# Kernel tuning notes

Hardware: AMD Instinct MI355X
Metric: run time of the kernel (lower is better)

Reference implementation:

```python
import jax, jax.numpy as jnp
import numpy as np

H = 256  # hidden_size


def _lstm_cell(x, h, c, Wih, Whh, b):
    # PyTorch gate order: input, forget, cell(g), output
    gates = x @ Wih.T + h @ Whh.T + b  # (B, 4H)
    i, f, g, o = jnp.split(gates, 4, axis=-1)
    c_new = jax.nn.sigmoid(f) * c + jax.nn.sigmoid(i) * jnp.tanh(g)
    h_new = jax.nn.sigmoid(o) * jnp.tanh(c_new)
    return h_new, c_new


def setup_inputs() -> dict:
    key = jax.random.key(0)
    ks = jax.random.split(key, 9)
    B, D_in, T, H4 = 64, 64, 1024, 4 * H
    s = 0.05  # keep gates out of saturation
    return {
        "x": jax.random.normal(ks[0], (B, D_in, T), jnp.float32),
        # layer 0: input size 64; layers 1-2: input size 2*H (bidirectional concat)
        "Wih0": jax.random.normal(ks[1], (2, H4, D_in), jnp.float32) * s,
        "Whh0": jax.random.normal(ks[2], (2, H4, H), jnp.float32) * s,
        "b0": jax.random.normal(ks[3], (2, H4), jnp.float32) * s,  # b_ih + b_hh fused
        "Wih12": jax.random.normal(ks[4], (2, 2, H4, 2 * H), jnp.float32) * s,
        "Whh12": jax.random.normal(ks[5], (2, 2, H4, H), jnp.float32) * s,
        "b12": jax.random.normal(ks[6], (2, 2, H4), jnp.float32) * s,
        # Conv1d(1, 81, (256,1)) == per-timestep linear over the hidden dim
        "conv_w": jax.random.normal(ks[7], (81, H), jnp.float32) * s,
        "conv_b": jax.random.normal(ks[8], (81,), jnp.float32) * s,
    }


def reference(x, Wih0, Whh0, b0, Wih12, Whh12, b12, conv_w, conv_b):
    B = x.shape[0]
    seq = jnp.transpose(x, (2, 0, 1))  # (T, B, D_in) like x.permute(2,0,1)
    h0 = jnp.zeros((6, B, H), x.dtype)  # num_layers * num_directions = 6
    c0 = jnp.zeros((6, B, H), x.dtype)

    def step(carry, x_t):
        h, c = carry
        hs, cs = [], []
        inp = x_t  # single timestep fed to the (bi)LSTM: both dirs see the same input
        for l in range(3):
            outs = []
            for d in range(2):
                idx = 2 * l + d
                if l == 0:
                    Wih, Whh, b = Wih0[d], Whh0[d], b0[d]
                else:
                    Wih, Whh, b = Wih12[l - 1, d], Whh12[l - 1, d], b12[l - 1, d]
                hn, cn = _lstm_cell(inp, h[idx], c[idx], Wih, Whh, b)
                outs.append(hn)
                hs.append(hn)
                cs.append(cn)
            inp = jnp.concatenate(outs, axis=-1)  # (B, 2H) into next layer
        new_h = jnp.stack(hs)
        new_c = jnp.stack(cs)
        # h.view(L, 2, B, H)[-1, -1]: last layer, backward direction
        return (new_h, new_c), hs[-1]

    _, ys = jax.lax.scan(step, (h0, c0), seq)  # ys: (T, B, H)

    # y.permute(1,2,0).unsqueeze(1) -> conv (256,1) kernel -> squeeze(2):
    # logits[b, o, t] = sum_h conv_w[o, h] * ys[t, b, h] + conv_b[o]
    logits = jnp.einsum('tbh,oh->bot', ys, conv_w) + conv_b[None, :, None]
    probs = jax.nn.softmax(logits, axis=1)
    return jnp.argmax(probs, axis=1)  # (B, T) int
```

## Files before the change

kernel.cpp:

```cpp
#include <hip/hip_runtime.h>


#define H_ 256
#define B_ 64
#define T_ 1024
#define NBLK 256
#define NTHR 1024
#define HBUF 98304
#define NTICK 1026

#define OFF_GEN  0
#define OFF_ROOT 64
#define OFF_CNT  128
#define OFF_H    4096
#define OFF_XT   1048576
#define OFF_YS   17825792

__device__ __forceinline__ float sigf(float x) {
  return 1.0f / (1.0f + __expf(-x));
}
__device__ __forceinline__ float tanhf_(float x) {
  float e = __expf(-2.0f * fabsf(x));
  float r = (1.0f - e) / (1.0f + e);
  return x >= 0.0f ? r : -r;
}

__device__ __forceinline__ void llc_ld1(const float4* p, float4& r) {
  asm volatile(
      "global_load_dwordx4 %0, %1, off sc0 sc1\n\t"
      "s_waitcnt vmcnt(0)"
      : "=v"(r)
      : "v"(p)
      : "memory");
}
__device__ __forceinline__ void llc_ld4(const float4* p, float4& r0, float4& r1,
                                        float4& r2, float4& r3) {
  asm volatile(
      "global_load_dwordx4 %0, %4, off sc0 sc1\n\t"
      "global_load_dwordx4 %1, %4, off offset:1024 sc0 sc1\n\t"
      "global_load_dwordx4 %2, %4, off offset:2048 sc0 sc1\n\t"
      "global_load_dwordx4 %3, %4, off offset:3072 sc0 sc1\n\t"
      "s_waitcnt vmcnt(0)"
      : "=&v"(r0), "=&v"(r1), "=&v"(r2), "=&v"(r3)
      : "v"(p)
      : "memory");
}
__device__ __forceinline__ void llc_ld8(const float4* p, const float4* q,
                                        float4& r0, float4& r1, float4& r2,
                                        float4& r3, float4& r4, float4& r5,
                                        float4& r6, float4& r7) {
  asm volatile(
      "global_load_dwordx4 %0, %8, off sc0 sc1\n\t"
      "global_load_dwordx4 %1, %8, off offset:1024 sc0 sc1\n\t"
      "global_load_dwordx4 %2, %8, off offset:2048 sc0 sc1\n\t"
      "global_load_dwordx4 %3, %8, off offset:3072 sc0 sc1\n\t"
      "global_load_dwordx4 %4, %9, off sc0 sc1\n\t"
      "global_load_dwordx4 %5, %9, off offset:1024 sc0 sc1\n\t"
      "global_load_dwordx4 %6, %9, off offset:2048 sc0 sc1\n\t"
      "global_load_dwordx4 %7, %9, off offset:3072 sc0 sc1\n\t"
      "s_waitcnt vmcnt(0)"
      : "=&v"(r0), "=&v"(r1), "=&v"(r2), "=&v"(r3), "=&v"(r4), "=&v"(r5),
        "=&v"(r6), "=&v"(r7)
      : "v"(p), "v"(q)
      : "memory");
}
__device__ __forceinline__ void llc_st_f2(float* p, float2 v) {
  asm volatile("global_store_dwordx2 %0, %1, off sc0 sc1" ::"v"(p), "v"(v)
               : "memory");
}

__global__ __launch_bounds__(64) void transpose_x(const float* __restrict__ x,
                                                  float* __restrict__ xT) {
  __shared__ float tile[64][65];
  const int k = blockIdx.y;
  const int t0 = blockIdx.x * 64;
  const int lane = threadIdx.x;
  for (int bi = 0; bi < 64; ++bi)
    tile[bi][lane] = x[bi * 65536 + k * 1024 + t0 + lane];
  __syncthreads();
  for (int ti = 0; ti < 64; ++ti)
    xT[(size_t)(t0 + ti) * 4096 + (k >> 2) * 256 + lane * 4 + (k & 3)] =
        tile[lane][ti];
}

__device__ __forceinline__ void body8(float* __restrict__ acc, const float4 av,
                                      const float* __restrict__ wl,
                                      const int k4) {
  const float* wp = wl + (size_t)k4 * 32;
#pragma unroll
  for (int a = 0; a < 8; ++a) {
    float4 wq = *(const float4*)(wp + a * 4);
    acc[a] += wq.x * av.x + wq.y * av.y + wq.z * av.z + wq.w * av.w;
  }
}

__device__ __forceinline__ void runLLC(float* __restrict__ acc,
                                       const float4* __restrict__ bufbase,
                                       const int bufk4, const int wk4,
                                       const int n,
                                       const float* __restrict__ wl,
                                       const int lane) {
  const float4* p = bufbase + (size_t)bufk4 * 64 + lane;
  int k = 0;
  for (; k + 8 <= n; k += 8) {
    float4 v0, v1, v2, v3, v4, v5, v6, v7;
    llc_ld8(p, p + 256, v0, v1, v2, v3, v4, v5, v6, v7);
    p += 512;
    body8(acc, v0, wl, wk4 + k + 0);
    body8(acc, v1, wl, wk4 + k + 1);
    body8(acc, v2, wl, wk4 + k + 2);
    body8(acc, v3, wl, wk4 + k + 3);
    body8(acc, v4, wl, wk4 + k + 4);
    body8(acc, v5, wl, wk4 + k + 5);
    body8(acc, v6, wl, wk4 + k + 6);
    body8(acc, v7, wl, wk4 + k + 7);
  }
  for (; k + 4 <= n; k += 4) {
    float4 v0, v1, v2, v3;
    llc_ld4(p, v0, v1, v2, v3);
    p += 256;
    body8(acc, v0, wl, wk4 + k + 0);
    body8(acc, v1, wl, wk4 + k + 1);
    body8(acc, v2, wl, wk4 + k + 2);
    body8(acc, v3, wl, wk4 + k + 3);
  }
  for (; k < n; ++k) {
    float4 v;
    llc_ld1(p, v);
    p += 64;
    body8(acc, v, wl, wk4 + k);
  }
}

__device__ __forceinline__ void runCached(float* __restrict__ acc,
                                          const float4* __restrict__ bufbase,
                                          const int bufk4, const int wk4,
                                          const int n,
                                          const float* __restrict__ wl,
                                          const int lane) {
  const float4* p = bufbase + (size_t)bufk4 * 64 + lane;
  int k = 0;
  for (; k + 4 <= n; k += 4) {
    float4 v0 = p[0], v1 = p[64], v2 = p[128], v3 = p[192];
    p += 256;
    body8(acc, v0, wl, wk4 + k + 0);
    body8(acc, v1, wl, wk4 + k + 1);
    body8(acc, v2, wl, wk4 + k + 2);
    body8(acc, v3, wl, wk4 + k + 3);
  }
  for (; k < n; ++k) {
    float4 v = *p;
    p += 64;
    body8(acc, v, wl, wk4 + k);
  }
}

__global__ __launch_bounds__(NTHR, 1) void lstm_persistent(
    const float* __restrict__ Wih0, const float* __restrict__ Whh0,
    const float* __restrict__ b0, const float* __restrict__ Wih12,
    const float* __restrict__ Whh12, const float* __restrict__ b12, char* wsb) {
  unsigned* gen = (unsigned*)(wsb + OFF_GEN);
  unsigned* root = (unsigned*)(wsb + OFF_ROOT);
  float* hb = (float*)(wsb + OFF_H);
  const float* xT = (const float*)(wsb + OFF_XT);
  float* ys = (float*)(wsb + OFF_YS);

  __shared__ float red[16][64][12];
  __shared__ float cst[3][2][64];
  __shared__ float wlds[14848];
  __shared__ float blds[3][8];

  const int bid = blockIdx.x;
  const int tid = threadIdx.x;
  const int lane = tid & 63;
  const int w = __builtin_amdgcn_readfirstlane(tid >> 6);
  const int d = bid >> 7;
  const int u0 = (bid & 127) * 2;

  if (tid < 384) ((float*)cst)[tid] = 0.f;

  auto stage = [&](const float* wA, int wAs, const float* wB, int wBs,
                   int K4s, int NA4s, float* dst) {
    const int nq = K4s * 8;
    for (int idx = tid; idx < nq; idx += NTHR) {
      const int a = idx / K4s;
      const int k4 = idx - a * K4s;
      const int row = (a & 3) * 256 + u0 + (a >> 2);
      const float* src = (k4 < NA4s) ? (wA + (size_t)row * wAs + k4 * 4)
                                     : (wB + (size_t)row * wBs + (k4 - NA4s) * 4);
      float4 q = *(const float4*)src;
      *(float4*)(dst + ((size_t)k4 * 8 + a) * 4) = q;
    }
  };
  stage(Wih0 + (size_t)d * 65536, 64, Whh0 + (size_t)d * 262144, 256, 80, 16,
        wlds);
  stage(Wih12 + (size_t)d * 524288, 512, Whh12 + (size_t)d * 262144, 256, 192,
        128, wlds + 2560);
  stage(Wih12 + (size_t)(2 + d) * 524288, 512,
        Whh12 + (size_t)(2 + d) * 262144, 256, 192, 128, wlds + 8704);
  if (tid < 24) {
    const int cell = tid >> 3, a = tid & 7;
    const float* bb = (cell == 0) ? (b0 + d * 1024)
                                  : ((cell == 1) ? (b12 + d * 1024)
                                                 : (b12 + (2 + d) * 1024));
    blds[cell][a] = bb[(a & 3) * 256 + u0 + (a >> 2)];
  }
  __syncthreads();

  unsigned* mycnt = (unsigned*)(wsb + OFF_CNT + (size_t)(bid & 7) * 64);

  for (unsigned tick = 0; tick < NTICK; ++tick) {
    const float* R = hb + ((tick + 1) & 1) * HBUF;
    float* W = hb + (tick & 1) * HBUF;
    const float4* Rf4 = (const float4*)R;

    const bool has0 = tick < 1024;
    const bool has1 = tick >= 1 && tick < 1025;
    const bool has2 = tick >= 2;

    float acc[8] = {0.f, 0.f, 0.f, 0.f, 0.f, 0.f, 0.f, 0.f};

    if (w < 4) {
      if (has0) {
        if (w == 0) {
          runCached(acc, (const float4*)xT + (size_t)tick * 1024, 0, 0, 16,
                    wlds, lane);
          runLLC(acc, Rf4 + (size_t)d * 4096, 0, 16, 4, wlds, lane);
        } else {
          const int lo = 20 * w;
          runLLC(acc, Rf4 + (size_t)d * 4096, lo - 16, lo, 20, wlds, lane);
        }
      }
    } else if (w < 10) {
      if (has1) {
        const int wi = w - 4, lo = 32 * wi;
        if (wi < 4)
          runLLC(acc, Rf4, lo, lo, 32, wlds + 2560, lane);
        else
          runLLC(acc, Rf4 + (size_t)(2 + d) * 4096, lo - 128, lo, 32,
                 wlds + 2560, lane);
      }
    } else {
      if (has2) {
        const int wi = w - 10, lo = 32 * wi;
        if (wi < 4)
          runLLC(acc, Rf4 + (size_t)2 * 4096, lo, lo, 32, wlds + 8704, lane);
        else
          runLLC(acc, Rf4 + (size_t)(4 + d) * 4096, lo - 128, lo, 32,
                 wlds + 8704, lane);
      }
    }

    *(float4*)&red[w][lane][0] = make_float4(acc[0], acc[1], acc[2], acc[3]);
    *(float4*)&red[w][lane][4] = make_float4(acc[4], acc[5], acc[6], acc[7]);
    __syncthreads();

    if (tid < 192) {
      const int cell = tid >> 6, b = tid & 63;
      const bool present = (cell == 0) ? has0 : ((cell == 1) ? has1 : has2);
      if (present) {
        const int w0 = (cell == 0) ? 0 : ((cell == 1) ? 4 : 10);
        const int nw = (cell == 0) ? 4 : 6;
        float g0 = blds[cell][0], g1 = blds[cell][1], g2 = blds[cell][2],
              g3 = blds[cell][3], g4 = blds[cell][4], g5 = blds[cell][5],
              g6 = blds[cell][6], g7 = blds[cell][7];
        for (int ww = w0; ww < w0 + nw; ++ww) {
          const float4* rp = (const float4*)&red[ww][b][0];
          float4 s0 = rp[0], s1 = rp[1];
          g0 += s0.x; g1 += s0.y; g2 += s0.z; g3 += s0.w;
          g4 += s1.x; g5 += s1.y; g6 += s1.z; g7 += s1.w;
        }
        const float iv0 = sigf(g0), fv0 = sigf(g1), gv0 = tanhf_(g2),
                    ov0 = sigf(g3);
        const float iv1 = sigf(g4), fv1 = sigf(g5), gv1 = tanhf_(g6),
                    ov1 = sigf(g7);
        float c0 = fv0 * cst[cell][0][b] + iv0 * gv0;
        float c1 = fv1 * cst[cell][1][b] + iv1 * gv1;
        cst[cell][0][b] = c0;
        cst[cell][1][b] = c1;
        const float h0 = ov0 * tanhf_(c0), h1 = ov1 * tanhf_(c1);
        const int cellidx = (cell == 0) ? d : ((cell == 1) ? (2 + d) : (4 + d));
        float* hp =
            W + (size_t)cellidx * 16384 + (u0 >> 2) * 256 + b * 4 + (u0 & 3);
        llc_st_f2(hp, make_float2(h0, h1));
        if (cell == 2 && d == 1) {
          *(float2*)(ys + (size_t)((int)tick - 2) * 16384 + b * 256 + u0) =
              make_float2(h0, h1);
        }
      }
    }
    asm volatile("s_waitcnt vmcnt(0)" ::: "memory");
    __syncthreads();

    if (tid == 0) {
      unsigned old = __hip_atomic_fetch_add(mycnt, 1u, __ATOMIC_RELAXED,
                                            __HIP_MEMORY_SCOPE_AGENT);
      if (old == (tick + 1) * (NBLK / 8) - 1) {
        unsigned r = __hip_atomic_fetch_add(root, 1u, __ATOMIC_RELAXED,
                                            __HIP_MEMORY_SCOPE_AGENT);
        if (r == (tick + 1) * 8 - 1) {
          __hip_atomic_store(gen, tick + 1, __ATOMIC_RELAXED,
                             __HIP_MEMORY_SCOPE_AGENT);
        }
      }
      while (__hip_atomic_load(gen, __ATOMIC_RELAXED, __HIP_MEMORY_SCOPE_AGENT) <
             tick + 1) {
        __builtin_amdgcn_s_sleep(2);
      }
    }
    __syncthreads();
  }
}

__global__ __launch_bounds__(256) void conv_argmax(const float* __restrict__ yst,
                                                   const float* __restrict__ cw,
                                                   const float* __restrict__ cb,
                                                   int* __restrict__ out) {
  const int t = blockIdx.x;
  const int tid = threadIdx.x, lane = tid & 63, w = tid >> 6;
  const float* yrow = yst + (size_t)t * (B_ * H_) + lane * H_;
  float best = -3.4e38f;
  int bi = 0;
  for (int og = 0; og < 3; ++og) {
    float acc[8];
    int ov[8];
#pragma unroll
    for (int m = 0; m < 8; ++m) {
      int o = w + 32 * og + 4 * m;
      ov[m] = (o < 81) ? o : 80;
      acc[m] = (o < 81) ? cb[o] : -3.4e38f;
    }
    for (int uu = 0; uu < H_; uu += 4) {
      float4 y4 = *(const float4*)(yrow + uu);
#pragma unroll
      for (int m = 0; m < 8; ++m) {
        const float* wr = cw + ov[m] * H_ + uu;
        acc[m] += wr[0] * y4.x + wr[1] * y4.y + wr[2] * y4.z + wr[3] * y4.w;
      }
    }
#pragma unroll
    for (int m = 0; m < 8; ++m) {
      int o = w + 32 * og + 4 * m;
      if (o < 81 && acc[m] > best) {
        best = acc[m];
        bi = o;
      }
    }
  }
  __shared__ float sv[4][64];
  __shared__ int si[4][64];
  sv[w][lane] = best;
  si[w][lane] = bi;
  __syncthreads();
  if (tid < 64) {
    float bv = sv[0][tid];
    int bo = si[0][tid];
#pragma unroll
    for (int ww = 1; ww < 4; ++ww) {
      float v = sv[ww][tid];
      int o = si[ww][tid];
      if (v > bv || (v == bv && o < bo)) {
        bv = v;
        bo = o;
      }
    }
    out[tid * T_ + t] = bo;
  }
}

extern "C" void kernel_launch(void* const* d_in, const int* in_sizes, int n_in,
                              void* d_out, int out_size, void* d_ws,
                              size_t ws_size, hipStream_t stream) {
  const float* x = (const float*)d_in[0];
  const float* Wih0 = (const float*)d_in[1];
  const float* Whh0 = (const float*)d_in[2];
  const float* b0 = (const float*)d_in[3];
  const float* Wih12 = (const float*)d_in[4];
  const float* Whh12 = (const float*)d_in[5];
  const float* b12 = (const float*)d_in[6];
  const float* cw = (const float*)d_in[7];
  const float* cb = (const float*)d_in[8];
  int* out = (int*)d_out;
  char* wsb = (char*)d_ws;

  hipMemsetAsync(wsb, 0, OFF_H + 786432, stream);
  transpose_x<<<dim3(16, 64, 1), dim3(64, 1, 1), 0, stream>>>(
      x, (float*)(wsb + OFF_XT));
  lstm_persistent<<<dim3(NBLK, 1, 1), dim3(NTHR, 1, 1), 0, stream>>>(
      Wih0, Whh0, b0, Wih12, Whh12, b12, wsb);
  conv_argmax<<<dim3(T_, 1, 1), dim3(256, 1, 1), 0, stream>>>(
      (const float*)(wsb + OFF_YS), cw, cb, out);
}
```

Measured before the change: 16.13 ms.

## Split LSTM persistent kernel into 512 blocks of one hidden unit each

Each persistent block now owns one hidden unit per direction instead of two. That doubles the grid to 512 blocks of 512 threads (8 waves) and halves per-block LDS weights, reduction buffers and cell state. Waves get longer K-ranges per cell, and the hierarchical barrier moves to 16 sub-counters. The intent is more blocks resident across CUs for parallelism and less per-block reduction work. The cost is that every block re-reads the full h vectors from LLC each tick, doubling global read traffic, and the grid barrier now has more participants.

Result: slower. 17.36 ms (+7.6%).

```diff
diff --git a/kernel.cpp b/kernel.cpp
--- a/kernel.cpp
+++ b/kernel.cpp
@@ -4,8 +4,8 @@
 #define H_ 256
 #define B_ 64
 #define T_ 1024
-#define NBLK 256
-#define NTHR 1024
+#define NBLK 512
+#define NTHR 512
 #define HBUF 98304
 #define NTICK 1026
 
@@ -64,8 +64,8 @@
       : "v"(p), "v"(q)
       : "memory");
 }
-__device__ __forceinline__ void llc_st_f2(float* p, float2 v) {
-  asm volatile("global_store_dwordx2 %0, %1, off sc0 sc1" ::"v"(p), "v"(v)
+__device__ __forceinline__ void llc_st1_nd(float* p, float v) {
+  asm volatile("global_store_dword %0, %1, off sc0 sc1" ::"v"(p), "v"(v)
                : "memory");
 }
 
@@ -83,12 +83,12 @@
         tile[lane][ti];
 }
 
-__device__ __forceinline__ void body8(float* __restrict__ acc, const float4 av,
+__device__ __forceinline__ void body4(float* __restrict__ acc, const float4 av,
                                       const float* __restrict__ wl,
                                       const int k4) {
-  const float* wp = wl + (size_t)k4 * 32;
-#pragma unroll
-  for (int a = 0; a < 8; ++a) {
+  const float* wp = wl + (size_t)k4 * 16;
+#pragma unroll
+  for (int a = 0; a < 4; ++a) {
     float4 wq = *(const float4*)(wp + a * 4);
     acc[a] += wq.x * av.x + wq.y * av.y + wq.z * av.z + wq.w * av.w;
   }
@@ -106,29 +106,29 @@
     float4 v0, v1, v2, v3, v4, v5, v6, v7;
     llc_ld8(p, p + 256, v0, v1, v2, v3, v4, v5, v6, v7);
     p += 512;
-    body8(acc, v0, wl, wk4 + k + 0);
-    body8(acc, v1, wl, wk4 + k + 1);
-    body8(acc, v2, wl, wk4 + k + 2);
-    body8(acc, v3, wl, wk4 + k + 3);
-    body8(acc, v4, wl, wk4 + k + 4);
-    body8(acc, v5, wl, wk4 + k + 5);
-    body8(acc, v6, wl, wk4 + k + 6);
-    body8(acc, v7, wl, wk4 + k + 7);
+    body4(acc, v0, wl, wk4 + k + 0);
+    body4(acc, v1, wl, wk4 + k + 1);
+    body4(acc, v2, wl, wk4 + k + 2);
+    body4(acc, v3, wl, wk4 + k + 3);
+    body4(acc, v4, wl, wk4 + k + 4);
+    body4(acc, v5, wl, wk4 + k + 5);
+    body4(acc, v6, wl, wk4 + k + 6);
+    body4(acc, v7, wl, wk4 + k + 7);
   }
   for (; k + 4 <= n; k += 4) {
     float4 v0, v1, v2, v3;
     llc_ld4(p, v0, v1, v2, v3);
     p += 256;
-    body8(acc, v0, wl, wk4 + k + 0);
-    body8(acc, v1, wl, wk4 + k + 1);
-    body8(acc, v2, wl, wk4 + k + 2);
-    body8(acc, v3, wl, wk4 + k + 3);
+    body4(acc, v0, wl, wk4 + k + 0);
+    body4(acc, v1, wl, wk4 + k + 1);
+    body4(acc, v2, wl, wk4 + k + 2);
+    body4(acc, v3, wl, wk4 + k + 3);
   }
   for (; k < n; ++k) {
     float4 v;
     llc_ld1(p, v);
     p += 64;
-    body8(acc, v, wl, wk4 + k);
+    body4(acc, v, wl, wk4 + k);
   }
 }
 
@@ -143,19 +143,19 @@
   for (; k + 4 <= n; k += 4) {
     float4 v0 = p[0], v1 = p[64], v2 = p[128], v3 = p[192];
     p += 256;
-    body8(acc, v0, wl, wk4 + k + 0);
-    body8(acc, v1, wl, wk4 + k + 1);
-    body8(acc, v2, wl, wk4 + k + 2);
-    body8(acc, v3, wl, wk4 + k + 3);
+    body4(acc, v0, wl, wk4 + k + 0);
+    body4(acc, v1, wl, wk4 + k + 1);
+    body4(acc, v2, wl, wk4 + k + 2);
+    body4(acc, v3, wl, wk4 + k + 3);
   }
   for (; k < n; ++k) {
     float4 v = *p;
     p += 64;
-    body8(acc, v, wl, wk4 + k);
-  }
-}
-
-__global__ __launch_bounds__(NTHR, 1) void lstm_persistent(
+    body4(acc, v, wl, wk4 + k);
+  }
+}
+
+__global__ __launch_bounds__(NTHR, 4) void lstm_persistent(
     const float* __restrict__ Wih0, const float* __restrict__ Whh0,
     const float* __restrict__ b0, const float* __restrict__ Wih12,
     const float* __restrict__ Whh12, const float* __restrict__ b12, char* wsb) {
@@ -165,49 +165,49 @@
   const float* xT = (const float*)(wsb + OFF_XT);
   float* ys = (float*)(wsb + OFF_YS);
 
-  __shared__ float red[16][64][12];
-  __shared__ float cst[3][2][64];
-  __shared__ float wlds[14848];
-  __shared__ float blds[3][8];
+  __shared__ float red[8][64][4];
+  __shared__ float cst[3][64];
+  __shared__ float wlds[7424];
+  __shared__ float blds[3][4];
 
   const int bid = blockIdx.x;
   const int tid = threadIdx.x;
   const int lane = tid & 63;
   const int w = __builtin_amdgcn_readfirstlane(tid >> 6);
-  const int d = bid >> 7;
-  const int u0 = (bid & 127) * 2;
-
-  if (tid < 384) ((float*)cst)[tid] = 0.f;
+  const int d = bid >> 8;
+  const int u = bid & 255;
+
+  if (tid < 192) ((float*)cst)[tid] = 0.f;
 
   auto stage = [&](const float* wA, int wAs, const float* wB, int wBs,
                    int K4s, int NA4s, float* dst) {
-    const int nq = K4s * 8;
+    const int nq = K4s * 4;
     for (int idx = tid; idx < nq; idx += NTHR) {
       const int a = idx / K4s;
       const int k4 = idx - a * K4s;
-      const int row = (a & 3) * 256 + u0 + (a >> 2);
+      const int row = a * 256 + u;
       const float* src = (k4 < NA4s) ? (wA + (size_t)row * wAs + k4 * 4)
                                      : (wB + (size_t)row * wBs + (k4 - NA4s) * 4);
       float4 q = *(const float4*)src;
-      *(float4*)(dst + ((size_t)k4 * 8 + a) * 4) = q;
+      *(float4*)(dst + ((size_t)k4 * 4 + a) * 4) = q;
     }
   };
   stage(Wih0 + (size_t)d * 65536, 64, Whh0 + (size_t)d * 262144, 256, 80, 16,
         wlds);
   stage(Wih12 + (size_t)d * 524288, 512, Whh12 + (size_t)d * 262144, 256, 192,
-        128, wlds + 2560);
+        128, wlds + 1280);
   stage(Wih12 + (size_t)(2 + d) * 524288, 512,
-        Whh12 + (size_t)(2 + d) * 262144, 256, 192, 128, wlds + 8704);
-  if (tid < 24) {
-    const int cell = tid >> 3, a = tid & 7;
+        Whh12 + (size_t)(2 + d) * 262144, 256, 192, 128, wlds + 4352);
+  if (tid < 12) {
+    const int cell = tid >> 2, a = tid & 3;
     const float* bb = (cell == 0) ? (b0 + d * 1024)
                                   : ((cell == 1) ? (b12 + d * 1024)
                                                  : (b12 + (2 + d) * 1024));
-    blds[cell][a] = bb[(a & 3) * 256 + u0 + (a >> 2)];
+    blds[cell][a] = bb[a * 256 + u];
   }
   __syncthreads();
 
-  unsigned* mycnt = (unsigned*)(wsb + OFF_CNT + (size_t)(bid & 7) * 64);
+  unsigned* mycnt = (unsigned*)(wsb + OFF_CNT + (size_t)(bid & 15) * 64);
 
   for (unsigned tick = 0; tick < NTICK; ++tick) {
     const float* R = hb + ((tick + 1) & 1) * HBUF;
@@ -218,74 +218,65 @@
     const bool has1 = tick >= 1 && tick < 1025;
     const bool has2 = tick >= 2;
 
-    float acc[8] = {0.f, 0.f, 0.f, 0.f, 0.f, 0.f, 0.f, 0.f};
-
-    if (w < 4) {
+    float acc[4] = {0.f, 0.f, 0.f, 0.f};
+
+    if (w < 2) {
       if (has0) {
         if (w == 0) {
           runCached(acc, (const float4*)xT + (size_t)tick * 1024, 0, 0, 16,
                     wlds, lane);
-          runLLC(acc, Rf4 + (size_t)d * 4096, 0, 16, 4, wlds, lane);
+          runLLC(acc, Rf4 + (size_t)d * 4096, 0, 16, 24, wlds, lane);
         } else {
-          const int lo = 20 * w;
-          runLLC(acc, Rf4 + (size_t)d * 4096, lo - 16, lo, 20, wlds, lane);
+          runLLC(acc, Rf4 + (size_t)d * 4096, 24, 40, 40, wlds, lane);
         }
       }
-    } else if (w < 10) {
+    } else if (w < 5) {
       if (has1) {
-        const int wi = w - 4, lo = 32 * wi;
-        if (wi < 4)
-          runLLC(acc, Rf4, lo, lo, 32, wlds + 2560, lane);
+        const int wi = w - 2;
+        if (wi < 2)
+          runLLC(acc, Rf4, wi * 64, wi * 64, 64, wlds + 1280, lane);
         else
-          runLLC(acc, Rf4 + (size_t)(2 + d) * 4096, lo - 128, lo, 32,
-                 wlds + 2560, lane);
+          runLLC(acc, Rf4 + (size_t)(2 + d) * 4096, 0, 128, 64, wlds + 1280,
+                 lane);
       }
     } else {
       if (has2) {
-        const int wi = w - 10, lo = 32 * wi;
-        if (wi < 4)
-          runLLC(acc, Rf4 + (size_t)2 * 4096, lo, lo, 32, wlds + 8704, lane);
+        const int wi = w - 5;
+        if (wi < 2)
+          runLLC(acc, Rf4 + (size_t)2 * 4096, wi * 64, wi * 64, 64,
+                 wlds + 4352, lane);
         else
-          runLLC(acc, Rf4 + (size_t)(4 + d) * 4096, lo - 128, lo, 32,
-                 wlds + 8704, lane);
+          runLLC(acc, Rf4 + (size_t)(4 + d) * 4096, 0, 128, 64, wlds + 4352,
+                 lane);
       }
     }
 
     *(float4*)&red[w][lane][0] = make_float4(acc[0], acc[1], acc[2], acc[3]);
-    *(float4*)&red[w][lane][4] = make_float4(acc[4], acc[5], acc[6], acc[7]);
     __syncthreads();
 
     if (tid < 192) {
       const int cell = tid >> 6, b = tid & 63;
       const bool present = (cell == 0) ? has0 : ((cell == 1) ? has1 : has2);
       if (present) {
-        const int w0 = (cell == 0) ? 0 : ((cell == 1) ? 4 : 10);
-        const int nw = (cell == 0) ? 4 : 6;
+        const int w0c = (cell == 0) ? 0 : ((cell == 1) ? 2 : 5);
+        const int nw = (cell == 0) ? 2 : 3;
         float g0 = blds[cell][0], g1 = blds[cell][1], g2 = blds[cell][2],
-              g3 = blds[cell][3], g4 = blds[cell][4], g5 = blds[cell][5],
-              g6 = blds[cell][6], g7 = blds[cell][7];
-        for (int ww = w0; ww < w0 + nw; ++ww) {
-          const float4* rp = (const float4*)&red[ww][b][0];
-          float4 s0 = rp[0], s1 = rp[1];
-          g0 += s0.x; g1 += s0.y; g2 += s0.z; g3 += s0.w;
-          g4 += s1.x; g5 += s1.y; g6 += s1.z; g7 += s1.w;
+              g3 = blds[cell][3];
+        for (int ww = w0c; ww < w0c + nw; ++ww) {
+          float4 s = *(const float4*)&red[ww][b][0];
+          g0 += s.x; g1 += s.y; g2 += s.z; g3 += s.w;
         }
-        const float iv0 = sigf(g0), fv0 = sigf(g1), gv0 = tanhf_(g2),
-                    ov0 = sigf(g3);
-        const float iv1 = sigf(g4), fv1 = sigf(g5), gv1 = tanhf_(g6),
-                    ov1 = sigf(g7);
-        float c0 = fv0 * cst[cell][0][b] + iv0 * gv0;
-        float c1 = fv1 * cst[cell][1][b] + iv1 * gv1;
-        cst[cell][0][b] = c0;
-        cst[cell][1][b] = c1;
-        const float h0 = ov0 * tanhf_(c0), h1 = ov1 * tanhf_(c1);
+        const float iv = sigf(g0), fv = sigf(g1), gv = tanhf_(g2),
+                    ov = sigf(g3);
+        float c = fv * cst[cell][b] + iv * gv;
+        cst[cell][b] = c;
+        const float h = ov * tanhf_(c);
         const int cellidx = (cell == 0) ? d : ((cell == 1) ? (2 + d) : (4 + d));
         float* hp =
-            W + (size_t)cellidx * 16384 + (u0 >> 2) * 256 + b * 4 + (u0 & 3);
-        llc_st_f2(hp, make_float2(h0, h1));
+            W + (size_t)cellidx * 16384 + (u >> 2) * 256 + b * 4 + (u & 3);
+        llc_st1_nd(hp, h);
         if (cell == 2 && d == 1) {
-          *(float2*)(ys + (size_t)((int)tick - 2) * 16384 + b * 256 + u0) =
-              make_float2(h0, h1);
+          ys[(size_t)((int)tick - 2) * 16384 + b * 256 + u] = h;
         }
       }
     }
@@ -295,10 +286,10 @@
     if (tid == 0) {
       unsigned old = __hip_atomic_fetch_add(mycnt, 1u, __ATOMIC_RELAXED,
                                             __HIP_MEMORY_SCOPE_AGENT);
-      if (old == (tick + 1) * (NBLK / 8) - 1) {
+      if (old == (tick + 1) * (NBLK / 16) - 1) {
         unsigned r = __hip_atomic_fetch_add(root, 1u, __ATOMIC_RELAXED,
                                             __HIP_MEMORY_SCOPE_AGENT);
-        if (r == (tick + 1) * 8 - 1) {
+        if (r == (tick + 1) * 16 - 1) {
           __hip_atomic_store(gen, tick + 1, __ATOMIC_RELAXED,
                              __HIP_MEMORY_SCOPE_AGENT);
         }
```
